# Performance work log

Hardware: AMD Instinct MI355X
Metric: run time of the kernel (lower is better)

The kernel has to match this reference:

```python
import jax, jax.numpy as jnp
import numpy as np

M, K, N = 8192, 1024, 8192

def setup_inputs() -> dict:
    key = jax.random.key(0)
    k1, k2, k3, k4 = jax.random.split(key, 4)
    # a, b are int8-valued quantized tensors (stored as int32 per harness dtype set)
    a = jax.random.randint(k1, (M, K), 0, 127, dtype=jnp.int32)
    b = jax.random.randint(k2, (K, N), 0, 127, dtype=jnp.int32)
    alpha_row = jax.random.uniform(k3, (M, 1), dtype=jnp.float32)
    alpha_col = jax.random.uniform(k4, (1, N), dtype=jnp.float32)
    return {"a": a, "b": b, "alpha_row": alpha_row, "alpha_col": alpha_col}

def reference(a, b, alpha_row, alpha_col):
    # Faithful to TorchGemmA8W8.forward: upcast int8 operands to fp32,
    # matmul with fp32 accumulate, cast result to int8.
    # (alpha_row / alpha_col are accepted but unused in this variant.)
    x = jnp.matmul(a.astype(jnp.float32), b.astype(jnp.float32))  # [M, N] fp32
    return x.astype(jnp.int8)
```

## Files before the change

### kernel.cpp

```cpp
#include <hip/hip_runtime.h>
#include <stdint.h>

#define M_DIM 8192
#define N_DIM 8192
#define K_DIM 1024
#define BK    128

typedef int int4v __attribute__((ext_vector_type(4)));

__device__ __forceinline__ void gload16(const char* g, char* l) {
    __builtin_amdgcn_global_load_lds(
        (__attribute__((address_space(1))) void*)(void*)const_cast<char*>(g),
        (__attribute__((address_space(3))) void*)l,
        16, 0, 0);
}

__device__ __forceinline__ int sat8(int v) {
    v = v > 127 ? 127 : v;
    v = v < -128 ? -128 : v;
    return v;
}

__global__ __launch_bounds__(256) void pack_a_kernel(const int* __restrict__ a,
                                                     int* __restrict__ out) {
    int i = blockIdx.x * 256 + threadIdx.x;
    int4 v = ((const int4*)a)[i];
    out[i] = (v.x & 0xff) | ((v.y & 0xff) << 8) |
             ((v.z & 0xff) << 16) | ((v.w & 0xff) << 24);
}

__global__ __launch_bounds__(256) void pack_b_kernel(const int* __restrict__ b,
                                                     char* __restrict__ out) {
    __shared__ char tile[64][68];
    const int n0 = blockIdx.x * 64;
    const int k0 = blockIdx.y * 64;
    const int t  = threadIdx.x;
    const int tr  = t >> 4;
    const int tc4 = (t & 15) << 2;
#pragma unroll
    for (int j = 0; j < 4; ++j) {
        int row = tr + j * 16;
        int4 v = *(const int4*)&b[(size_t)(k0 + row) * N_DIM + n0 + tc4];
        tile[row][tc4 + 0] = (char)v.x;
        tile[row][tc4 + 1] = (char)v.y;
        tile[row][tc4 + 2] = (char)v.z;
        tile[row][tc4 + 3] = (char)v.w;
    }
    __syncthreads();
#pragma unroll
    for (int j = 0; j < 4; ++j) {
        int n = tr + j * 16;
        int pk = (tile[tc4 + 0][n] & 0xff) |
                 ((tile[tc4 + 1][n] & 0xff) << 8) |
                 ((tile[tc4 + 2][n] & 0xff) << 16) |
                 ((tile[tc4 + 3][n] & 0xff) << 24);
        *(int*)&out[(size_t)(n0 + n) * K_DIM + k0 + tc4] = pk;
    }
}

__global__ __launch_bounds__(256) void gemm_i8_kernel(const char* __restrict__ A8,
                                                      const char* __restrict__ B8,
                                                      int* __restrict__ C) {
    __shared__ __align__(16) char As[2 * 128 * 64];
    __shared__ __align__(16) char Bs[2 * 128 * 64];

    const int t    = threadIdx.x;
    const int bn   = blockIdx.x;
    const int bm   = blockIdx.y;
    const int lane = t & 63;
    const int wave = t >> 6;
    const int wm   = wave >> 1;
    const int wn   = wave & 1;
    const int quad = lane >> 4;
    const int l16  = lane & 15;

    const size_t aBase = (size_t)(bm * 128) * K_DIM;
    const size_t bBase = (size_t)(bn * 128) * K_DIM;

    const int sr = t >> 2;
    const int sc = (t & 3) << 4;

    int4v acc[4][4] = {};

    for (int kt = 0; kt < K_DIM / BK; ++kt) {
        const int kOff = kt * BK;
#pragma unroll
        for (int s = 0; s < 4; ++s) {
            const int p = s >> 1;
            const int r = ((s & 1) << 6) + sr;
            const int f = s * 4096 + t * 16;
            gload16(A8 + aBase + (size_t)r * K_DIM + kOff + p * 64 + sc, As + f);
            gload16(B8 + bBase + (size_t)r * K_DIM + kOff + p * 64 + sc, Bs + f);
        }
        __syncthreads();

#pragma unroll
        for (int h = 0; h < 2; ++h) {
            int4v af[4], bf[4];
#pragma unroll
            for (int mi = 0; mi < 4; ++mi)
                af[mi] = *(const int4v*)
                    &As[h * 8192 + (wm * 64 + mi * 16 + l16) * 64 + quad * 16];
#pragma unroll
            for (int ni = 0; ni < 4; ++ni)
                bf[ni] = *(const int4v*)
                    &Bs[h * 8192 + (wn * 64 + ni * 16 + l16) * 64 + quad * 16];

#pragma unroll
            for (int mi = 0; mi < 4; ++mi)
#pragma unroll
                for (int ni = 0; ni < 4; ++ni)
                    acc[mi][ni] = __builtin_amdgcn_mfma_i32_16x16x64_i8(
                        af[mi], bf[ni], acc[mi][ni], 0, 0, 0);
        }

        __syncthreads();
    }

    const int mBase = bm * 128 + wm * 64;
    const int nBase = bn * 128 + wn * 64;
#pragma unroll
    for (int mi = 0; mi < 4; ++mi) {
#pragma unroll
        for (int ni = 0; ni < 4; ++ni) {
            const int col = nBase + ni * 16 + l16;
#pragma unroll
            for (int r = 0; r < 4; ++r) {
                const int row = mBase + mi * 16 + quad * 4 + r;
                C[(size_t)row * N_DIM + col] = sat8(acc[mi][ni][r]);
            }
        }
    }
}

__global__ __launch_bounds__(256) void gemm_naive_kernel(const int* __restrict__ a,
                                                         const int* __restrict__ b,
                                                         int* __restrict__ C) {
    const int col = blockIdx.x * 256 + threadIdx.x;
    const int row = blockIdx.y;
    int acc = 0;
    for (int k = 0; k < K_DIM; ++k)
        acc += a[(size_t)row * K_DIM + k] * b[(size_t)k * N_DIM + col];
    C[(size_t)row * N_DIM + col] = sat8(acc);
}

extern "C" void kernel_launch(void* const* d_in, const int* in_sizes, int n_in,
                              void* d_out, int out_size, void* d_ws, size_t ws_size,
                              hipStream_t stream) {
    const int* a = (const int*)d_in[0];
    const int* b = (const int*)d_in[1];
    int* out = (int*)d_out;

    const size_t needed = 2 * (size_t)M_DIM * K_DIM;
    if (ws_size < needed) {
        gemm_naive_kernel<<<dim3(N_DIM / 256, M_DIM), 256, 0, stream>>>(a, b, out);
        return;
    }

    char* A8 = (char*)d_ws;
    char* B8 = A8 + (size_t)M_DIM * K_DIM;

    pack_a_kernel<<<(M_DIM * K_DIM / 4) / 256, 256, 0, stream>>>(a, (int*)A8);
    pack_b_kernel<<<dim3(N_DIM / 64, K_DIM / 64), 256, 0, stream>>>(b, B8);
    gemm_i8_kernel<<<dim3(N_DIM / 128, M_DIM / 128), 256, 0, stream>>>(A8, B8, out);
}
```

Measured before the change: 366.1 us.

## Load A fragments directly to registers with prefetch, enlarge block tile to 256x128

The GEMM kernel no longer stages A in LDS. Each wave owns 64 rows of A and loads its MFMA fragments straight from global memory into registers, prefetching the next K tile while computing the current one. The block tile grows to 256x128, with each wave computing a 64x128 strip against the shared B tile. This halves LDS traffic and doubles reuse of B per block, at the cost of more accumulator registers (32 int4 accumulators, with a 2-blocks-per-CU launch bound) and uncoalesced 16-byte strided global loads for A.

```diff
diff --git a/kernel.cpp b/kernel.cpp
--- a/kernel.cpp
+++ b/kernel.cpp
@@ -58,10 +58,9 @@
     }
 }
 
-__global__ __launch_bounds__(256) void gemm_i8_kernel(const char* __restrict__ A8,
-                                                      const char* __restrict__ B8,
-                                                      int* __restrict__ C) {
-    __shared__ __align__(16) char As[2 * 128 * 64];
+__global__ __launch_bounds__(256, 2) void gemm_i8_kernel(const char* __restrict__ A8,
+                                                         const char* __restrict__ B8,
+                                                         int* __restrict__ C) {
     __shared__ __align__(16) char Bs[2 * 128 * 64];
 
     const int t    = threadIdx.x;
@@ -69,64 +68,79 @@
     const int bm   = blockIdx.y;
     const int lane = t & 63;
     const int wave = t >> 6;
-    const int wm   = wave >> 1;
-    const int wn   = wave & 1;
     const int quad = lane >> 4;
     const int l16  = lane & 15;
 
-    const size_t aBase = (size_t)(bm * 128) * K_DIM;
+    const int    mWave = bm * 256 + wave * 64;
+    const char*  aPtr  = A8 + (size_t)(mWave + l16) * K_DIM + quad * 16;
     const size_t bBase = (size_t)(bn * 128) * K_DIM;
 
     const int sr = t >> 2;
     const int sc = (t & 3) << 4;
 
-    int4v acc[4][4] = {};
+    int4v acc[4][8] = {};
+
+    int4v af[2][4];
+#pragma unroll
+    for (int h = 0; h < 2; ++h)
+#pragma unroll
+        for (int mi = 0; mi < 4; ++mi)
+            af[h][mi] = *(const int4v*)(aPtr + (size_t)mi * 16 * K_DIM + h * 64);
 
     for (int kt = 0; kt < K_DIM / BK; ++kt) {
         const int kOff = kt * BK;
+
 #pragma unroll
         for (int s = 0; s < 4; ++s) {
-            const int p = s >> 1;
             const int r = ((s & 1) << 6) + sr;
             const int f = s * 4096 + t * 16;
-            gload16(A8 + aBase + (size_t)r * K_DIM + kOff + p * 64 + sc, As + f);
-            gload16(B8 + bBase + (size_t)r * K_DIM + kOff + p * 64 + sc, Bs + f);
+            gload16(B8 + bBase + (size_t)r * K_DIM + kOff + (s >> 1) * 64 + sc,
+                    Bs + f);
         }
         __syncthreads();
 
+        const int kNext = (kt < K_DIM / BK - 1) ? kOff + BK : 0;
+        int4v afn[2][4];
+#pragma unroll
+        for (int h = 0; h < 2; ++h)
+#pragma unroll
+            for (int mi = 0; mi < 4; ++mi)
+                afn[h][mi] = *(const int4v*)(aPtr + (size_t)mi * 16 * K_DIM +
+                                             kNext + h * 64);
+
 #pragma unroll
         for (int h = 0; h < 2; ++h) {
-            int4v af[4], bf[4];
+            int4v bf[8];
 #pragma unroll
-            for (int mi = 0; mi < 4; ++mi)
-                af[mi] = *(const int4v*)
-                    &As[h * 8192 + (wm * 64 + mi * 16 + l16) * 64 + quad * 16];
-#pragma unroll
-            for (int ni = 0; ni < 4; ++ni)
-                bf[ni] = *(const int4v*)
-                    &Bs[h * 8192 + (wn * 64 + ni * 16 + l16) * 64 + quad * 16];
-
+            for (int ni = 0; ni < 8; ++ni)
+                bf[ni] = *(const int4v*)&Bs[h * 8192 + (ni * 16 + l16) * 64 +
+                                            quad * 16];
 #pragma unroll
             for (int mi = 0; mi < 4; ++mi)
 #pragma unroll
-                for (int ni = 0; ni < 4; ++ni)
+                for (int ni = 0; ni < 8; ++ni)
                     acc[mi][ni] = __builtin_amdgcn_mfma_i32_16x16x64_i8(
-                        af[mi], bf[ni], acc[mi][ni], 0, 0, 0);
+                        af[h][mi], bf[ni], acc[mi][ni], 0, 0, 0);
         }
 
         __syncthreads();
+
+#pragma unroll
+        for (int h = 0; h < 2; ++h)
+#pragma unroll
+            for (int mi = 0; mi < 4; ++mi)
+                af[h][mi] = afn[h][mi];
     }
 
-    const int mBase = bm * 128 + wm * 64;
-    const int nBase = bn * 128 + wn * 64;
+    const int nB0 = bn * 128;
 #pragma unroll
     for (int mi = 0; mi < 4; ++mi) {
 #pragma unroll
-        for (int ni = 0; ni < 4; ++ni) {
-            const int col = nBase + ni * 16 + l16;
+        for (int ni = 0; ni < 8; ++ni) {
+            const int col = nB0 + ni * 16 + l16;
 #pragma unroll
             for (int r = 0; r < 4; ++r) {
-                const int row = mBase + mi * 16 + quad * 4 + r;
+                const int row = mWave + mi * 16 + quad * 4 + r;
                 C[(size_t)row * N_DIM + col] = sat8(acc[mi][ni][r]);
             }
         }
@@ -162,5 +176,5 @@
 
     pack_a_kernel<<<(M_DIM * K_DIM / 4) / 256, 256, 0, stream>>>(a, (int*)A8);
     pack_b_kernel<<<dim3(N_DIM / 64, K_DIM / 64), 256, 0, stream>>>(b, B8);
-    gemm_i8_kernel<<<dim3(N_DIM / 128, M_DIM / 128), 256, 0, stream>>>(A8, B8, out);
+    gemm_i8_kernel<<<dim3(N_DIM / 128, M_DIM / 256), 256, 0, stream>>>(A8, B8, out);
 }
```

Measured after the change: 381.4 us. 1.04x slower.

## Merge pack kernels and remap GEMM tiles for XCD-local L2 reuse

Applied to the files above, without the earlier changes.

Combines the A and B packing kernels into one launch by dispatching on block index, which removes one kernel launch and the gap between the two. The GEMM grid becomes 1D, and block IDs are remapped so that blocks sent round-robin to the same XCD share a narrow band of B columns. This is meant to raise L2 hit rates for B tiles. The remap hardcodes a grid of 64x64 tiles and assumes eight XCDs with round-robin dispatch.

```diff
diff --git a/kernel.cpp b/kernel.cpp
--- a/kernel.cpp
+++ b/kernel.cpp
@@ -21,20 +21,22 @@
     return v;
 }
 
-__global__ __launch_bounds__(256) void pack_a_kernel(const int* __restrict__ a,
-                                                     int* __restrict__ out) {
-    int i = blockIdx.x * 256 + threadIdx.x;
-    int4 v = ((const int4*)a)[i];
-    out[i] = (v.x & 0xff) | ((v.y & 0xff) << 8) |
-             ((v.z & 0xff) << 16) | ((v.w & 0xff) << 24);
-}
-
-__global__ __launch_bounds__(256) void pack_b_kernel(const int* __restrict__ b,
-                                                     char* __restrict__ out) {
+__global__ __launch_bounds__(256) void pack_ab_kernel(const int* __restrict__ a,
+                                                      const int* __restrict__ b,
+                                                      int* __restrict__ outA,
+                                                      char* __restrict__ outB) {
     __shared__ char tile[64][68];
-    const int n0 = blockIdx.x * 64;
-    const int k0 = blockIdx.y * 64;
-    const int t  = threadIdx.x;
+    const int t = threadIdx.x;
+    if (blockIdx.x < 8192) {
+        int i = blockIdx.x * 256 + t;
+        int4 v = ((const int4*)a)[i];
+        outA[i] = (v.x & 0xff) | ((v.y & 0xff) << 8) |
+                  ((v.z & 0xff) << 16) | ((v.w & 0xff) << 24);
+        return;
+    }
+    const int bx = blockIdx.x - 8192;
+    const int n0 = (bx & 127) * 64;
+    const int k0 = (bx >> 7) * 64;
     const int tr  = t >> 4;
     const int tc4 = (t & 15) << 2;
 #pragma unroll
@@ -54,7 +56,7 @@
                  ((tile[tc4 + 1][n] & 0xff) << 8) |
                  ((tile[tc4 + 2][n] & 0xff) << 16) |
                  ((tile[tc4 + 3][n] & 0xff) << 24);
-        *(int*)&out[(size_t)(n0 + n) * K_DIM + k0 + tc4] = pk;
+        *(int*)&outB[(size_t)(n0 + n) * K_DIM + k0 + tc4] = pk;
     }
 }
 
@@ -64,9 +66,13 @@
     __shared__ __align__(16) char As[2 * 128 * 64];
     __shared__ __align__(16) char Bs[2 * 128 * 64];
 
+    const int lin = blockIdx.x;
+    const int xcd = lin & 7;
+    const int r   = lin >> 3;
+    const int bn  = xcd * 8 + (r >> 6);
+    const int bm  = r & 63;
+
     const int t    = threadIdx.x;
-    const int bn   = blockIdx.x;
-    const int bm   = blockIdx.y;
     const int lane = t & 63;
     const int wave = t >> 6;
     const int wm   = wave >> 1;
@@ -87,10 +93,10 @@
 #pragma unroll
         for (int s = 0; s < 4; ++s) {
             const int p = s >> 1;
-            const int r = ((s & 1) << 6) + sr;
+            const int rr = ((s & 1) << 6) + sr;
             const int f = s * 4096 + t * 16;
-            gload16(A8 + aBase + (size_t)r * K_DIM + kOff + p * 64 + sc, As + f);
-            gload16(B8 + bBase + (size_t)r * K_DIM + kOff + p * 64 + sc, Bs + f);
+            gload16(A8 + aBase + (size_t)rr * K_DIM + kOff + p * 64 + sc, As + f);
+            gload16(B8 + bBase + (size_t)rr * K_DIM + kOff + p * 64 + sc, Bs + f);
         }
         __syncthreads();
 
@@ -125,9 +131,9 @@
         for (int ni = 0; ni < 4; ++ni) {
             const int col = nBase + ni * 16 + l16;
 #pragma unroll
-            for (int r = 0; r < 4; ++r) {
-                const int row = mBase + mi * 16 + quad * 4 + r;
-                C[(size_t)row * N_DIM + col] = sat8(acc[mi][ni][r]);
+            for (int r2 = 0; r2 < 4; ++r2) {
+                const int row = mBase + mi * 16 + quad * 4 + r2;
+                C[(size_t)row * N_DIM + col] = sat8(acc[mi][ni][r2]);
             }
         }
     }
@@ -160,7 +166,6 @@
     char* A8 = (char*)d_ws;
     char* B8 = A8 + (size_t)M_DIM * K_DIM;
 
-    pack_a_kernel<<<(M_DIM * K_DIM / 4) / 256, 256, 0, stream>>>(a, (int*)A8);
-    pack_b_kernel<<<dim3(N_DIM / 64, K_DIM / 64), 256, 0, stream>>>(b, B8);
-    gemm_i8_kernel<<<dim3(N_DIM / 128, M_DIM / 128), 256, 0, stream>>>(A8, B8, out);
+    pack_ab_kernel<<<8192 + 2048, 256, 0, stream>>>(a, b, (int*)A8, B8);
+    gemm_i8_kernel<<<4096, 256, 0, stream>>>(A8, B8, out);
 }
```

After: 426.5 us. +16.5%, slower.
